# Kernel tuning notes

Measured on AMD Instinct MI355X. Metric: run time of the kernel, lower is better.

The kernel has to match this reference:

```python
import jax, jax.numpy as jnp
import numpy as np

DIM = 1024
HEADS = 16
B, N = 4, 2048


def setup_inputs() -> dict:
    key = jax.random.key(0)
    ks = jax.random.split(key, 6)
    scale = DIM ** -0.5
    return {
        "x": jax.random.normal(ks[0], (B, N, DIM), dtype=jnp.float32),
        "mask": jax.random.randint(ks[1], (B, N, N), 0, 2) > 0,
        "Wqkv": jax.random.normal(ks[2], (DIM, 3 * DIM), dtype=jnp.float32) * scale,
        "bqkv": jax.random.normal(ks[3], (3 * DIM,), dtype=jnp.float32) * 0.02,
        "Wproj": jax.random.normal(ks[4], (DIM, DIM), dtype=jnp.float32) * scale,
        "bproj": jax.random.normal(ks[5], (DIM,), dtype=jnp.float32) * 0.02,
    }


def reference(x, mask, Wqkv, bqkv, Wproj, bproj):
    Bs, Ns, C = x.shape
    H = HEADS
    D = C // H
    scale = D ** -0.5
    qkv = x @ Wqkv + bqkv                       # [B, N, 3C]
    qkv = qkv.reshape(Bs, Ns, 3, H, D)          # split (three h d)
    q, k, v = jnp.moveaxis(qkv, 2, 0)           # each [B, N, H, D]
    q = q.transpose(0, 2, 1, 3)                 # [B, H, N, D]
    k = k.transpose(0, 2, 1, 3)
    v = v.transpose(0, 2, 1, 3)
    attn = jnp.einsum("bhnd,bhmd->bhnm", q, k) * scale  # [B, H, N, N]
    attn = jnp.where(mask[:, None, :, :], -jnp.inf, attn)
    attn = jax.nn.softmax(attn, axis=-1)
    out = jnp.einsum("bhnm,bhmd->bhnd", attn, v)        # [B, H, N, D]
    out = out.transpose(0, 2, 1, 3).reshape(Bs, Ns, C)  # [B, N, C]
    return out @ Wproj + bproj
```

## Files before the change

kernel.cpp:

```cpp
#include <hip/hip_runtime.h>
#include <cstdint>
#include <cstddef>

constexpr int kC = 1024;
constexpr int kH = 16;
constexpr int kB = 4;
constexpr int kN = 2048;
constexpr int kD = 64;

typedef unsigned short u16;
typedef unsigned int   u32;
typedef unsigned long long u64;
typedef __bf16 v8bf  __attribute__((ext_vector_type(8)));
typedef float  v4f   __attribute__((ext_vector_type(4)));
typedef u16    u16x8 __attribute__((ext_vector_type(8)));
typedef u16    u16x4 __attribute__((ext_vector_type(4)));

__device__ inline u16 f2bf(float f) {
    union { float f; unsigned u; } v; v.f = f;
    unsigned r = v.u + 0x7FFFu + ((v.u >> 16) & 1u);
    return (u16)(r >> 16);
}

__device__ inline void gl2lds16(const u16* g, u16* l) {
    __builtin_amdgcn_global_load_lds(
        (const __attribute__((address_space(1))) void*)g,
        (__attribute__((address_space(3))) void*)l, 16, 0, 0);
}

__global__ __launch_bounds__(256) void cast_bf16_kernel(
    const float* __restrict__ in, u16* __restrict__ outp)
{
    const int i = blockIdx.x * 256 + threadIdx.x;
    const float4 f = ((const float4*)in)[i];
    u16x4 o;
    o.x = f2bf(f.x); o.y = f2bf(f.y); o.z = f2bf(f.z); o.w = f2bf(f.w);
    ((u16x4*)outp)[i] = o;
}

__global__ __launch_bounds__(256) void tpose_cast_kernel(
    const float* __restrict__ W, u16* __restrict__ Wt, int R, int Cc)
{
    __shared__ u16 tile[64][65];
    const int c0 = blockIdx.x * 64;
    const int r0 = blockIdx.y * 64;
    const int t  = threadIdx.x;
#pragma unroll
    for (int it = 0; it < 16; ++it) {
        const int r = it * 4 + (t >> 6);
        const int c = t & 63;
        tile[c][r] = f2bf(W[(size_t)(r0 + r) * Cc + c0 + c]);
    }
    __syncthreads();
#pragma unroll
    for (int it = 0; it < 16; ++it) {
        const int rr = it * 4 + (t >> 6);
        const int cc = t & 63;
        Wt[(size_t)(c0 + rr) * R + r0 + cc] = tile[rr][cc];
    }
}

__global__ __launch_bounds__(256) void maskpack_kernel(
    const int* __restrict__ mask, u32* __restrict__ bits)
{
    const int seg  = blockIdx.x * 4 + (threadIdx.x >> 6);
    const int lane = threadIdx.x & 63;
    const size_t row = (size_t)(seg >> 5);
    const int s = seg & 31;
    const int m = mask[row * kN + s * 64 + lane];
    const u64 bal = __ballot(m != 0);
    if (lane == 0) ((u64*)bits)[row * 32 + s] = bal;
}

template <int MODE>
__global__ __launch_bounds__(256) void gemm_mfma_kernel(
    const u16* __restrict__ A, const u16* __restrict__ Bt,
    const float* __restrict__ bias, float* __restrict__ Cout,
    u16* __restrict__ qOut, u16* __restrict__ kOut, u16* __restrict__ vOut,
    int M, int N, int K)
{
    __shared__ u16 As[128 * 32];
    __shared__ u16 Bs[128 * 32];
    const int t    = threadIdx.x;
    const int w    = t >> 6;
    const int lane = t & 63;
    const int quad = lane >> 4;
    const int l16  = lane & 15;
    const int m0   = blockIdx.y * 128;
    const int n0   = blockIdx.x * 128;

    const int sr = lane >> 2;
    const int sk = (lane & 3) * 8;
    const u16* Ag0 = A  + (size_t)(m0 + 32 * w      + sr) * K + sk;
    const u16* Ag1 = A  + (size_t)(m0 + 32 * w + 16 + sr) * K + sk;
    const u16* Bg0 = Bt + (size_t)(n0 + 32 * w      + sr) * K + sk;
    const u16* Bg1 = Bt + (size_t)(n0 + 32 * w + 16 + sr) * K + sk;
    u16* Al0 = &As[(32 * w)      * 32];
    u16* Al1 = &As[(32 * w + 16) * 32];
    u16* Bl0 = &Bs[(32 * w)      * 32];
    u16* Bl1 = &Bs[(32 * w + 16) * 32];

    v4f acc[4][4];
#pragma unroll
    for (int r = 0; r < 4; ++r)
#pragma unroll
        for (int c = 0; c < 4; ++c) acc[r][c] = (v4f){0.f, 0.f, 0.f, 0.f};

    const int mrow = (w >> 1) * 64;
    const int ncol = (w & 1) * 64;

    for (int k0 = 0; k0 < K; k0 += 32) {
        __syncthreads();
        gl2lds16(Ag0 + k0, Al0);
        gl2lds16(Ag1 + k0, Al1);
        gl2lds16(Bg0 + k0, Bl0);
        gl2lds16(Bg1 + k0, Bl1);
        __syncthreads();

        v8bf af[4], bfr[4];
#pragma unroll
        for (int r = 0; r < 4; ++r)
            af[r] = *(const v8bf*)(&As[(mrow + r * 16 + l16) * 32 + quad * 8]);
#pragma unroll
        for (int c = 0; c < 4; ++c)
            bfr[c] = *(const v8bf*)(&Bs[(ncol + c * 16 + l16) * 32 + quad * 8]);
#pragma unroll
        for (int r = 0; r < 4; ++r)
#pragma unroll
            for (int c = 0; c < 4; ++c)
                acc[r][c] = __builtin_amdgcn_mfma_f32_16x16x32_bf16(
                    af[r], bfr[c], acc[r][c], 0, 0, 0);
    }

#pragma unroll
    for (int r = 0; r < 4; ++r) {
#pragma unroll
        for (int c = 0; c < 4; ++c) {
            const int col = n0 + ncol + c * 16 + l16;
            const float bv = bias[col];
#pragma unroll
            for (int reg = 0; reg < 4; ++reg) {
                const int row = m0 + mrow + r * 16 + quad * 4 + reg;
                const float val = acc[r][c][reg] + bv;
                if (MODE == 0) {
                    Cout[(size_t)row * N + col] = val;
                } else {
                    const int which = col >> 10;
                    const int rem   = col & 1023;
                    const int h     = rem >> 6;
                    const int d     = rem & 63;
                    const int b     = row >> 11;
                    const int n     = row & 2047;
                    u16* dst = (which == 0) ? qOut : (which == 1) ? kOut : vOut;
                    dst[(((size_t)(b * kH + h)) * kN + n) * kD + d] = f2bf(val);
                }
            }
        }
    }
}

__global__ __launch_bounds__(256, 3) void attn_mfma_kernel(
    const u16* __restrict__ q, const u16* __restrict__ k,
    const u16* __restrict__ v, const u32* __restrict__ mbits,
    u16* __restrict__ out)
{
    __shared__ u16 Ks[128 * 64];
    __shared__ u16 Vt[64 * 128];
    __shared__ u16 Ps[64 * 128];

    const int t    = threadIdx.x;
    const int w    = t >> 6;
    const int lane = t & 63;
    const int quad = lane >> 4;
    const int l16  = lane & 15;

    const int bh    = blockIdx.x >> 5;
    const int tile0 = (blockIdx.x & 31) * 64;
    const int b     = bh >> 4;
    const int h     = bh & 15;

    const u16* qb = q + (size_t)bh * kN * kD;
    const u16* kb = k + (size_t)bh * kN * kD;
    const u16* vb = v + (size_t)bh * kN * kD;

    const int qrow = tile0 + w * 16 + l16;
    const v8bf qf0 = *(const v8bf*)(qb + (size_t)qrow * kD + quad * 8);
    const v8bf qf1 = *(const v8bf*)(qb + (size_t)qrow * kD + 32 + quad * 8);

    const u32* mrowb = mbits + ((size_t)b * kN + qrow) * 64;

    const int skr  = t >> 1;
    const int skh  = t & 1;
    const int svk  = t >> 3;
    const int svd  = t & 7;
    const u16* kgp = kb + (size_t)skr * kD + skh * 32;
    const u16* vgp = vb + (size_t)(svk * 4) * kD + svd * 8;

    u16x8 kpre[4], vpre[4];
    uint4 mpre;
    auto prefetch = [&](int k0) {
        const u16x8* ks = (const u16x8*)(kgp + (size_t)k0 * kD);
        kpre[0] = ks[0]; kpre[1] = ks[1]; kpre[2] = ks[2]; kpre[3] = ks[3];
        const u16* vs = vgp + (size_t)k0 * kD;
        vpre[0] = *(const u16x8*)(vs);
        vpre[1] = *(const u16x8*)(vs + kD);
        vpre[2] = *(const u16x8*)(vs + 2 * kD);
        vpre[3] = *(const u16x8*)(vs + 3 * kD);
        mpre = *(const uint4*)(mrowb + (k0 >> 5));
    };

    v4f oacc[4];
#pragma unroll
    for (int i = 0; i < 4; ++i) oacc[i] = (v4f){0.f, 0.f, 0.f, 0.f};
    float rs = 0.f;

    prefetch(0);

    for (int kt = 0; kt < kN / 128; ++kt) {
        u16x8 kcur[4], vcur[4];
#pragma unroll
        for (int i = 0; i < 4; ++i) { kcur[i] = kpre[i]; vcur[i] = vpre[i]; }
        const uint4 mcur = mpre;
        const u32 mw[4] = {mcur.x, mcur.y, mcur.z, mcur.w};
        if (kt + 1 < kN / 128) prefetch((kt + 1) * 128);

        __syncthreads();

        {
            const int cb = skh * 4;
            u16* drow = &Ks[skr * 64];
#pragma unroll
            for (int i = 0; i < 4; ++i)
                *(u16x8*)(&drow[((cb + i) ^ (skr & 7)) * 8]) = kcur[i];
        }
        {
            const int blk = svk >> 1;
            const int off = (svk & 1) * 4;
#pragma unroll
            for (int j = 0; j < 8; ++j) {
                const int d = svd * 8 + j;
                u16x4 p;
                p.x = vcur[0][j]; p.y = vcur[1][j]; p.z = vcur[2][j]; p.w = vcur[3][j];
                *(u16x4*)(&Vt[d * 128 + ((blk ^ (d & 15)) * 8) + off]) = p;
            }
        }
        __syncthreads();

#pragma unroll
        for (int nb = 0; nb < 8; ++nb) {
            const int krow = nb * 16 + l16;
            const v8bf kf0 = *(const v8bf*)(&Ks[krow * 64 + ((quad       ^ (krow & 7)) * 8)]);
            const v8bf kf1 = *(const v8bf*)(&Ks[krow * 64 + (((quad + 4) ^ (krow & 7)) * 8)]);
            v4f s = (v4f){0.f, 0.f, 0.f, 0.f};
            s = __builtin_amdgcn_mfma_f32_16x16x32_bf16(kf0, qf0, s, 0, 0, 0);
            s = __builtin_amdgcn_mfma_f32_16x16x32_bf16(kf1, qf1, s, 0, 0, 0);

            const u32 m4 = (mw[nb >> 1] >> ((nb & 1) * 16 + quad * 4)) & 0xFu;
            const float e0 = (m4 & 1u) ? 0.f : __expf(s[0] * 0.125f);
            const float e1 = (m4 & 2u) ? 0.f : __expf(s[1] * 0.125f);
            const float e2 = (m4 & 4u) ? 0.f : __expf(s[2] * 0.125f);
            const float e3 = (m4 & 8u) ? 0.f : __expf(s[3] * 0.125f);
            rs += (e0 + e1) + (e2 + e3);

            u16x4 pw; pw.x = f2bf(e0); pw.y = f2bf(e1); pw.z = f2bf(e2); pw.w = f2bf(e3);
            const int pblk = nb * 2 + (quad >> 1);
            *(u16x4*)(&Ps[(w * 16 + l16) * 128 + ((pblk ^ l16) * 8) + (quad & 1) * 4]) = pw;
        }

#pragma unroll
        for (int ks = 0; ks < 4; ++ks) {
            const v8bf pa = *(const v8bf*)(&Ps[(w * 16 + l16) * 128 + (((ks * 4 + quad) ^ l16) * 8)]);
#pragma unroll
            for (int db = 0; db < 4; ++db) {
                const int d = db * 16 + l16;
                const v8bf vf = *(const v8bf*)(&Vt[d * 128 + (((ks * 4 + quad) ^ (d & 15)) * 8)]);
                oacc[db] = __builtin_amdgcn_mfma_f32_16x16x32_bf16(pa, vf, oacc[db], 0, 0, 0);
            }
        }
    }

    rs += __shfl_xor(rs, 16);
    rs += __shfl_xor(rs, 32);
    const float inv = 1.f / rs;
    float rq[4];
#pragma unroll
    for (int reg = 0; reg < 4; ++reg)
        rq[reg] = __shfl(inv, quad * 4 + reg);

#pragma unroll
    for (int db = 0; db < 4; ++db) {
#pragma unroll
        for (int reg = 0; reg < 4; ++reg) {
            const int row = tile0 + w * 16 + quad * 4 + reg;
            const int col = h * 64 + db * 16 + l16;
            out[((size_t)(b * kN + row)) * kC + col] = f2bf(oacc[db][reg] * rq[reg]);
        }
    }
}

extern "C" void kernel_launch(void* const* d_in, const int* in_sizes, int n_in,
                              void* d_out, int out_size, void* d_ws, size_t ws_size,
                              hipStream_t stream)
{
    const float* x     = (const float*)d_in[0];
    const int*   mask  = (const int*)d_in[1];
    const float* Wqkv  = (const float*)d_in[2];
    const float* bqkv  = (const float*)d_in[3];
    const float* Wproj = (const float*)d_in[4];
    const float* bproj = (const float*)d_in[5];
    float* out = (float*)d_out;

    const size_t nx = (size_t)kB * kN * kC;
    const size_t qkv_elems = (size_t)kB * kH * kN * kD;
    u16* xb     = (u16*)d_ws;
    u16* qbuf   = xb + nx;
    u16* kbuf   = qbuf + qkv_elems;
    u16* vbuf   = kbuf + qkv_elems;
    u16* aob    = vbuf + qkv_elems;
    u16* Wqkvt  = aob + nx;
    u16* Wprojt = Wqkvt + (size_t)3 * kC * kC;
    u32* mbits  = (u32*)(Wprojt + (size_t)kC * kC);

    maskpack_kernel<<<dim3(kB * kN * 32 / 4), dim3(256), 0, stream>>>(mask, mbits);
    cast_bf16_kernel<<<dim3(nx / 1024), dim3(256), 0, stream>>>(x, xb);
    tpose_cast_kernel<<<dim3(3 * kC / 64, kC / 64), dim3(256), 0, stream>>>(
        Wqkv, Wqkvt, kC, 3 * kC);
    tpose_cast_kernel<<<dim3(kC / 64, kC / 64), dim3(256), 0, stream>>>(
        Wproj, Wprojt, kC, kC);

    gemm_mfma_kernel<1><<<dim3(3 * kC / 128, kB * kN / 128), dim3(256), 0, stream>>>(
        xb, Wqkvt, bqkv, nullptr, qbuf, kbuf, vbuf, kB * kN, 3 * kC, kC);

    attn_mfma_kernel<<<dim3(kB * kH * (kN / 64)), dim3(256), 0, stream>>>(
        qbuf, kbuf, vbuf, mbits, aob);

    gemm_mfma_kernel<0><<<dim3(kC / 128, kB * kN / 128), dim3(256), 0, stream>>>(
        aob, Wprojt, bproj, out, nullptr, nullptr, nullptr, kB * kN, kC, kC);
}
```

Before: 444.2 us.

## Fold softmax scale into Q, use exp2, restructure V transpose, add setprio

The QKV projection epilogue now premultiplies Q by scale*log2(e), so the attention loop can call a native exp2 instead of scaling and calling __expf. The V staging is reorganised so each thread loads eight rows of four elements and writes full 16-byte columns to the transposed LDS tile instead of 8-byte pieces. P values are converted to bf16 with the compiler cast instead of the manual rounding helper. Wave priority is raised around the PV MFMA block. These changes cut VALU work in the softmax and LDS store count, at the cost of more, smaller global loads for V.

```diff
diff --git a/kernel.cpp b/kernel.cpp
--- a/kernel.cpp
+++ b/kernel.cpp
@@ -8,10 +8,13 @@
 constexpr int kN = 2048;
 constexpr int kD = 64;
 
+#define KQ_SCALE 0.18033688011112042f
+
 typedef unsigned short u16;
 typedef unsigned int   u32;
 typedef unsigned long long u64;
 typedef __bf16 v8bf  __attribute__((ext_vector_type(8)));
+typedef __bf16 v4bf  __attribute__((ext_vector_type(4)));
 typedef float  v4f   __attribute__((ext_vector_type(4)));
 typedef u16    u16x8 __attribute__((ext_vector_type(8)));
 typedef u16    u16x4 __attribute__((ext_vector_type(4)));
@@ -20,6 +23,14 @@
     union { float f; unsigned u; } v; v.f = f;
     unsigned r = v.u + 0x7FFFu + ((v.u >> 16) & 1u);
     return (u16)(r >> 16);
+}
+
+__device__ inline float fast_exp2(float x) {
+#if __has_builtin(__builtin_amdgcn_exp2f)
+    return __builtin_amdgcn_exp2f(x);
+#else
+    return __expf(x * 0.6931471805599453f);
+#endif
 }
 
 __device__ inline void gl2lds16(const u16* g, u16* l) {
@@ -141,7 +152,7 @@
 #pragma unroll
             for (int reg = 0; reg < 4; ++reg) {
                 const int row = m0 + mrow + r * 16 + quad * 4 + reg;
-                const float val = acc[r][c][reg] + bv;
+                float val = acc[r][c][reg] + bv;
                 if (MODE == 0) {
                     Cout[(size_t)row * N + col] = val;
                 } else {
@@ -151,6 +162,7 @@
                     const int d     = rem & 63;
                     const int b     = row >> 11;
                     const int n     = row & 2047;
+                    if (which == 0) val *= KQ_SCALE;
                     u16* dst = (which == 0) ? qOut : (which == 1) ? kOut : vOut;
                     dst[(((size_t)(b * kH + h)) * kN + n) * kD + d] = f2bf(val);
                 }
@@ -191,21 +203,21 @@
 
     const int skr  = t >> 1;
     const int skh  = t & 1;
-    const int svk  = t >> 3;
-    const int svd  = t & 7;
+    const int vg   = t >> 4;
+    const int vdq  = t & 15;
     const u16* kgp = kb + (size_t)skr * kD + skh * 32;
-    const u16* vgp = vb + (size_t)(svk * 4) * kD + svd * 8;
-
-    u16x8 kpre[4], vpre[4];
+    const u16* vgp = vb + (size_t)(vg * 8) * kD + vdq * 4;
+
+    u16x8 kpre[4];
+    u16x4 vpre[8];
     uint4 mpre;
     auto prefetch = [&](int k0) {
         const u16x8* ks = (const u16x8*)(kgp + (size_t)k0 * kD);
         kpre[0] = ks[0]; kpre[1] = ks[1]; kpre[2] = ks[2]; kpre[3] = ks[3];
         const u16* vs = vgp + (size_t)k0 * kD;
-        vpre[0] = *(const u16x8*)(vs);
-        vpre[1] = *(const u16x8*)(vs + kD);
-        vpre[2] = *(const u16x8*)(vs + 2 * kD);
-        vpre[3] = *(const u16x8*)(vs + 3 * kD);
+#pragma unroll
+        for (int i = 0; i < 8; ++i)
+            vpre[i] = *(const u16x4*)(vs + (size_t)i * kD);
         mpre = *(const uint4*)(mrowb + (k0 >> 5));
     };
 
@@ -217,9 +229,12 @@
     prefetch(0);
 
     for (int kt = 0; kt < kN / 128; ++kt) {
-        u16x8 kcur[4], vcur[4];
-#pragma unroll
-        for (int i = 0; i < 4; ++i) { kcur[i] = kpre[i]; vcur[i] = vpre[i]; }
+        u16x8 kcur[4];
+        u16x4 vcur[8];
+#pragma unroll
+        for (int i = 0; i < 4; ++i) kcur[i] = kpre[i];
+#pragma unroll
+        for (int i = 0; i < 8; ++i) vcur[i] = vpre[i];
         const uint4 mcur = mpre;
         const u32 mw[4] = {mcur.x, mcur.y, mcur.z, mcur.w};
         if (kt + 1 < kN / 128) prefetch((kt + 1) * 128);
@@ -234,14 +249,13 @@
                 *(u16x8*)(&drow[((cb + i) ^ (skr & 7)) * 8]) = kcur[i];
         }
         {
-            const int blk = svk >> 1;
-            const int off = (svk & 1) * 4;
-#pragma unroll
-            for (int j = 0; j < 8; ++j) {
-                const int d = svd * 8 + j;
-                u16x4 p;
-                p.x = vcur[0][j]; p.y = vcur[1][j]; p.z = vcur[2][j]; p.w = vcur[3][j];
-                *(u16x4*)(&Vt[d * 128 + ((blk ^ (d & 15)) * 8) + off]) = p;
+#pragma unroll
+            for (int dd = 0; dd < 4; ++dd) {
+                const int d = vdq * 4 + dd;
+                u16x8 col;
+#pragma unroll
+                for (int j = 0; j < 8; ++j) col[j] = vcur[j][dd];
+                *(u16x8*)(&Vt[d * 128 + ((vg ^ (d & 15)) * 8)]) = col;
             }
         }
         __syncthreads();
@@ -256,17 +270,22 @@
             s = __builtin_amdgcn_mfma_f32_16x16x32_bf16(kf1, qf1, s, 0, 0, 0);
 
             const u32 m4 = (mw[nb >> 1] >> ((nb & 1) * 16 + quad * 4)) & 0xFu;
-            const float e0 = (m4 & 1u) ? 0.f : __expf(s[0] * 0.125f);
-            const float e1 = (m4 & 2u) ? 0.f : __expf(s[1] * 0.125f);
-            const float e2 = (m4 & 4u) ? 0.f : __expf(s[2] * 0.125f);
-            const float e3 = (m4 & 8u) ? 0.f : __expf(s[3] * 0.125f);
+            float e0 = fast_exp2(s[0]);
+            float e1 = fast_exp2(s[1]);
+            float e2 = fast_exp2(s[2]);
+            float e3 = fast_exp2(s[3]);
+            e0 = (m4 & 1u) ? 0.f : e0;
+            e1 = (m4 & 2u) ? 0.f : e1;
+            e2 = (m4 & 4u) ? 0.f : e2;
+            e3 = (m4 & 8u) ? 0.f : e3;
             rs += (e0 + e1) + (e2 + e3);
 
-            u16x4 pw; pw.x = f2bf(e0); pw.y = f2bf(e1); pw.z = f2bf(e2); pw.w = f2bf(e3);
+            v4bf pw = {(__bf16)e0, (__bf16)e1, (__bf16)e2, (__bf16)e3};
             const int pblk = nb * 2 + (quad >> 1);
-            *(u16x4*)(&Ps[(w * 16 + l16) * 128 + ((pblk ^ l16) * 8) + (quad & 1) * 4]) = pw;
-        }
-
+            *(v4bf*)(&Ps[(w * 16 + l16) * 128 + ((pblk ^ l16) * 8) + (quad & 1) * 4]) = pw;
+        }
+
+        __builtin_amdgcn_s_setprio(1);
 #pragma unroll
         for (int ks = 0; ks < 4; ++ks) {
             const v8bf pa = *(const v8bf*)(&Ps[(w * 16 + l16) * 128 + (((ks * 4 + quad) ^ l16) * 8)]);
@@ -277,6 +296,7 @@
                 oacc[db] = __builtin_amdgcn_mfma_f32_16x16x32_bf16(pa, vf, oacc[db], 0, 0, 0);
             }
         }
+        __builtin_amdgcn_s_setprio(0);
     }
 
     rs += __shfl_xor(rs, 16);
```

Result: faster. 403.3 us (-9.2%).
